# Kernel optimization log

Measured on AMD Instinct MI355X. Metric: run time of the kernel, lower is better.

Reference implementation:

```python
import jax, jax.numpy as jnp
import numpy as np

B, D, H = 8192, 512, 512


def _linear_init(key, out_dim, in_dim, bias=True):
    # torch nn.Linear default: U(-1/sqrt(in_dim), 1/sqrt(in_dim)) for W and b
    k1, k2 = jax.random.split(key)
    bound = 1.0 / np.sqrt(in_dim)
    W = jax.random.uniform(k1, (out_dim, in_dim), jnp.float32, -bound, bound)
    if not bias:
        return W
    b = jax.random.uniform(k2, (out_dim,), jnp.float32, -bound, bound)
    return W, b


def setup_inputs() -> dict:
    key = jax.random.key(0)
    ks = jax.random.split(key, 16)
    x = jax.random.normal(ks[0], (B, D), jnp.float32)
    delta_t = jax.random.uniform(ks[1], (B, 1), jnp.float32)
    hidden = jax.random.normal(ks[2], (B, H), jnp.float32)
    cell_s = jax.random.normal(ks[3], (B, H), jnp.float32)
    Wii, bii = _linear_init(ks[4], H, D)
    Whi, bhi = _linear_init(ks[5], H, H)
    Wig, big = _linear_init(ks[6], H, D)
    Whg, bhg = _linear_init(ks[7], H, H)
    Wio, bio = _linear_init(ks[8], H, D)
    Who, bho = _linear_init(ks[9], H, H)
    Wto, bto = _linear_init(ks[10], H, 1)
    Wco, bco = _linear_init(ks[11], H, H)
    Wit1, bit1 = _linear_init(ks[12], H, D)
    Wtt1 = _linear_init(ks[13], H, 1, bias=False)
    Wit2, bit2 = _linear_init(ks[14], H, D)
    Wtt2 = _linear_init(ks[15], H, 1, bias=False)
    return dict(x=x, delta_t=delta_t, hidden=hidden, cell_s=cell_s,
                Wii=Wii, bii=bii, Whi=Whi, bhi=bhi, Wig=Wig, big=big,
                Whg=Whg, bhg=bhg, Wio=Wio, bio=bio, Who=Who, bho=bho,
                Wto=Wto, bto=bto, Wco=Wco, bco=bco, Wit1=Wit1, bit1=bit1,
                Wtt1=Wtt1, Wit2=Wit2, bit2=bit2, Wtt2=Wtt2)


def _lin(a, W, b=None):
    y = a @ W.T
    return y if b is None else y + b


def reference(x, delta_t, hidden, cell_s,
              Wii, bii, Whi, bhi, Wig, big, Whg, bhg,
              Wio, bio, Who, bho, Wto, bto, Wco, bco,
              Wit1, bit1, Wtt1, Wit2, bit2, Wtt2):
    sig, tanh = jax.nn.sigmoid, jnp.tanh
    tm1 = sig(_lin(x, Wit1, bit1) + sig(_lin(delta_t, Wtt1)))
    tm2 = sig(_lin(x, Wit2, bit2) + sig(_lin(delta_t, Wtt2)))
    im = sig(_lin(x, Wii, bii) + _lin(hidden, Whi, bhi))
    cur_in = tanh(_lin(x, Wig, big) + _lin(hidden, Whg, bhg))
    it1 = im * tm1
    cm_t = (1.0 - it1) * cell_s + it1 * cur_in
    cm = (1.0 - im) * cell_s + im * tm2 * cur_in
    om = sig(_lin(x, Wio, bio) + _lin(delta_t, Wto, bto)
             + _lin(hidden, Who, bho) + _lin(cm_t, Wco, bco))
    hm = om * tanh(cm_t)
    return (hm, cm)
```

## Files before the change

kernel.cpp:

```cpp
#include <hip/hip_runtime.h>
#include <hip/hip_bf16.h>
#include <stdint.h>

#define B_SZ 8192
#define D_SZ 512
#define H_SZ 512
#define KC 1024
#define NPRE 2560
#define PRE_LD 2560

typedef __attribute__((ext_vector_type(8))) __bf16 bf16x8;
typedef __attribute__((ext_vector_type(4))) float f32x4;

__device__ __forceinline__ unsigned short f2bf(float f) {
  unsigned u = __builtin_bit_cast(unsigned, f);
  u += 0x7FFFu + ((u >> 16) & 1u);
  return (unsigned short)(u >> 16);
}
__device__ __forceinline__ float bf2f(unsigned short h) {
  unsigned u = ((unsigned)h) << 16;
  return __builtin_bit_cast(float, u);
}
__device__ __forceinline__ float sigf(float x) { return 1.0f / (1.0f + __expf(-x)); }

__device__ __forceinline__ void async_ld16(const unsigned short* g, unsigned short* l) {
  __builtin_amdgcn_global_load_lds(
      (const __attribute__((address_space(1))) unsigned int*)g,
      (__attribute__((address_space(3))) unsigned int*)l, 16, 0, 0);
}

struct WSrcs { const float* wx[5]; const float* wh[3]; const float* wco; };

__global__ void pack_all(const float* __restrict__ x, const float* __restrict__ h, WSrcs ws,
                         unsigned short* __restrict__ Ab, unsigned short* __restrict__ Wall,
                         unsigned short* __restrict__ Wcob) {
  int i = (blockIdx.x * 256 + threadIdx.x) * 4;
  const int XH = B_SZ * KC;
  const float* s;
  unsigned short* d;
  if (i < XH) {
    int b = i >> 10, c = i & 1023;
    s = (c < 512) ? (x + (size_t)b * 512 + c) : (h + (size_t)b * 512 + (c - 512));
    d = Ab + i;
  } else if (i < XH + NPRE * KC) {
    int j = i - XH;
    int row = j >> 10, c = j & 1023;
    int gate = row >> 9, r = row & 511;
    d = Wall + j;
    if (c < 512) {
      s = ws.wx[gate] + (size_t)r * 512 + c;
    } else if (gate >= 2) {
      s = ws.wh[gate - 2] + (size_t)r * 512 + (c - 512);
    } else {
      *(ushort4*)d = (ushort4){0, 0, 0, 0};
      return;
    }
  } else {
    int j = i - XH - NPRE * KC;
    s = ws.wco + j;
    d = Wcob + j;
  }
  float4 v = *(const float4*)s;
  ushort4 o; o.x = f2bf(v.x); o.y = f2bf(v.y); o.z = f2bf(v.z); o.w = f2bf(v.w);
  *(ushort4*)d = o;
}

__global__ __launch_bounds__(256, 2) void gemm_bt(
    const unsigned short* __restrict__ A, const unsigned short* __restrict__ W,
    unsigned short* __restrict__ C, int K, int ldc) {
  __shared__ bf16x8 sA[128 * 8];
  __shared__ bf16x8 sW[128 * 8];
  const int tid  = threadIdx.x;
  const int wave = tid >> 6, lane = tid & 63;
  const int ln15 = lane & 15, kq = lane >> 4;
  const int wr = wave >> 1, wc = wave & 1;
  const long bm = (long)blockIdx.y * 128;
  const long bn = (long)blockIdx.x * 128;

  f32x4 acc[4][4];
#pragma unroll
  for (int i = 0; i < 4; ++i)
#pragma unroll
    for (int j = 0; j < 4; ++j) acc[i][j] = (f32x4){0.f, 0.f, 0.f, 0.f};

  const int nK = (bn < 1024) ? (512 >> 6) : (K >> 6);
  const int swb = ln15 & 7;

  for (int kt = 0; kt < nK; ++kt) {
    const int k0 = kt << 6;
    __syncthreads();
#pragma unroll
    for (int it = 0; it < 4; ++it) {
      int f   = it * 256 + tid;
      int row = f >> 3;
      int col = ((f & 7) ^ (row & 7)) << 3;
      int ldsc = it * 256 + wave * 64;
      async_ld16(A + (size_t)(bm + row) * K + k0 + col, (unsigned short*)sA + (size_t)ldsc * 8);
      async_ld16(W + (size_t)(bn + row) * K + k0 + col, (unsigned short*)sW + (size_t)ldsc * 8);
    }
    __syncthreads();
#pragma unroll
    for (int ko = 0; ko < 2; ++ko) {
      const int q = (ko * 4 + kq) ^ swb;
      bf16x8 af[4], wf[4];
#pragma unroll
      for (int t = 0; t < 4; ++t)
        af[t] = sA[(wr * 64 + t * 16 + ln15) * 8 + q];
#pragma unroll
      for (int t = 0; t < 4; ++t)
        wf[t] = sW[(wc * 64 + t * 16 + ln15) * 8 + q];
#pragma unroll
      for (int i = 0; i < 4; ++i)
#pragma unroll
        for (int j = 0; j < 4; ++j)
          acc[i][j] = __builtin_amdgcn_mfma_f32_16x16x32_bf16(af[i], wf[j], acc[i][j], 0, 0, 0);
    }
  }
#pragma unroll
  for (int i = 0; i < 4; ++i) {
    const long r0 = bm + wr * 64 + i * 16 + kq * 4;
#pragma unroll
    for (int j = 0; j < 4; ++j) {
      const long c = bn + wc * 64 + j * 16 + ln15;
#pragma unroll
      for (int r = 0; r < 4; ++r)
        C[(size_t)(r0 + r) * ldc + c] = f2bf(acc[i][j][r]);
    }
  }
}

__global__ void gate_kernel(unsigned short* __restrict__ Pre,
                            const float* __restrict__ delta_t, const float* __restrict__ cell_s,
                            const float* __restrict__ bii, const float* __restrict__ bhi,
                            const float* __restrict__ big, const float* __restrict__ bhg,
                            const float* __restrict__ bio, const float* __restrict__ bho,
                            const float* __restrict__ Wto, const float* __restrict__ bto,
                            const float* __restrict__ bco,
                            const float* __restrict__ bit1, const float* __restrict__ Wtt1,
                            const float* __restrict__ bit2, const float* __restrict__ Wtt2,
                            float* __restrict__ out_cm, unsigned short* __restrict__ cmt_b) {
  int i4 = (blockIdx.x * 256 + threadIdx.x) * 4;
  int b = i4 >> 9, h = i4 & 511;
  size_t p = (size_t)b * PRE_LD;
  float dt = delta_t[b];
  ushort4 u1 = *(const ushort4*)(Pre + p + h);
  ushort4 u2 = *(const ushort4*)(Pre + p + 512 + h);
  ushort4 ui = *(const ushort4*)(Pre + p + 1024 + h);
  ushort4 ug = *(const ushort4*)(Pre + p + 1536 + h);
  ushort4 uo = *(const ushort4*)(Pre + p + 2048 + h);
  float4 cs  = *(const float4*)(cell_s + i4);
  float4 vbii = *(const float4*)(bii + h),  vbhi = *(const float4*)(bhi + h);
  float4 vbig = *(const float4*)(big + h),  vbhg = *(const float4*)(bhg + h);
  float4 vbio = *(const float4*)(bio + h),  vbho = *(const float4*)(bho + h);
  float4 vWto = *(const float4*)(Wto + h),  vbto = *(const float4*)(bto + h);
  float4 vbco = *(const float4*)(bco + h);
  float4 vbt1 = *(const float4*)(bit1 + h), vwt1 = *(const float4*)(Wtt1 + h);
  float4 vbt2 = *(const float4*)(bit2 + h), vwt2 = *(const float4*)(Wtt2 + h);

  float4 ocm; ushort4 ocmt; ushort4 oao;
  const unsigned short* pu1 = (const unsigned short*)&u1;
  const unsigned short* pu2 = (const unsigned short*)&u2;
  const unsigned short* pui = (const unsigned short*)&ui;
  const unsigned short* pug = (const unsigned short*)&ug;
  const unsigned short* puo = (const unsigned short*)&uo;
  const float* pcs = (const float*)&cs;
  float* pocm = (float*)&ocm;
  unsigned short* pocmt = (unsigned short*)&ocmt;
  unsigned short* poao = (unsigned short*)&oao;
#pragma unroll
  for (int l = 0; l < 4; ++l) {
    float a1 = bf2f(pu1[l]) + ((const float*)&vbt1)[l];
    float a2 = bf2f(pu2[l]) + ((const float*)&vbt2)[l];
    float ai = bf2f(pui[l]) + ((const float*)&vbii)[l] + ((const float*)&vbhi)[l];
    float ag = bf2f(pug[l]) + ((const float*)&vbig)[l] + ((const float*)&vbhg)[l];
    float ao = bf2f(puo[l]) + ((const float*)&vbio)[l] + ((const float*)&vbho)[l]
             + dt * ((const float*)&vWto)[l] + ((const float*)&vbto)[l] + ((const float*)&vbco)[l];
    float t1 = sigf(a1 + sigf(dt * ((const float*)&vwt1)[l]));
    float t2 = sigf(a2 + sigf(dt * ((const float*)&vwt2)[l]));
    float im = sigf(ai);
    float g  = tanhf(ag);
    float csl = pcs[l];
    float it1 = im * t1;
    float cmt = (1.f - it1) * csl + it1 * g;
    float cm  = (1.f - im) * csl + im * t2 * g;
    pocm[l]  = cm;
    pocmt[l] = f2bf(cmt);
    poao[l]  = f2bf(ao);
  }
  *(float4*)(out_cm + i4) = ocm;
  *(ushort4*)(cmt_b + i4) = ocmt;
  *(ushort4*)(Pre + p + 2048 + h) = oao;
}

__global__ __launch_bounds__(256, 2) void gemm_out(
    const unsigned short* __restrict__ A , const unsigned short* __restrict__ W ,
    const unsigned short* __restrict__ Pre, float* __restrict__ out_hm) {
  __shared__ bf16x8 sA[128 * 8];
  __shared__ bf16x8 sW[128 * 8];
  const int tid  = threadIdx.x;
  const int wave = tid >> 6, lane = tid & 63;
  const int ln15 = lane & 15, kq = lane >> 4;
  const int wr = wave >> 1, wc = wave & 1;
  const long bm = (long)blockIdx.y * 128;
  const long bn = (long)blockIdx.x * 128;
  const int K = H_SZ;
  const int swb = ln15 & 7;

  f32x4 acc[4][4];
#pragma unroll
  for (int i = 0; i < 4; ++i)
#pragma unroll
    for (int j = 0; j < 4; ++j) acc[i][j] = (f32x4){0.f, 0.f, 0.f, 0.f};

  for (int kt = 0; kt < (K >> 6); ++kt) {
    const int k0 = kt << 6;
    __syncthreads();
#pragma unroll
    for (int it = 0; it < 4; ++it) {
      int f   = it * 256 + tid;
      int row = f >> 3;
      int col = ((f & 7) ^ (row & 7)) << 3;
      int ldsc = it * 256 + wave * 64;
      async_ld16(A + (size_t)(bm + row) * K + k0 + col, (unsigned short*)sA + (size_t)ldsc * 8);
      async_ld16(W + (size_t)(bn + row) * K + k0 + col, (unsigned short*)sW + (size_t)ldsc * 8);
    }
    __syncthreads();
#pragma unroll
    for (int ko = 0; ko < 2; ++ko) {
      const int q = (ko * 4 + kq) ^ swb;
      bf16x8 af[4], wf[4];
#pragma unroll
      for (int t = 0; t < 4; ++t)
        af[t] = sA[(wr * 64 + t * 16 + ln15) * 8 + q];
#pragma unroll
      for (int t = 0; t < 4; ++t)
        wf[t] = sW[(wc * 64 + t * 16 + ln15) * 8 + q];
#pragma unroll
      for (int i = 0; i < 4; ++i)
#pragma unroll
        for (int j = 0; j < 4; ++j)
          acc[i][j] = __builtin_amdgcn_mfma_f32_16x16x32_bf16(af[i], wf[j], acc[i][j], 0, 0, 0);
    }
  }
#pragma unroll
  for (int i = 0; i < 4; ++i) {
    const long r0 = bm + wr * 64 + i * 16 + kq * 4;
#pragma unroll
    for (int j = 0; j < 4; ++j) {
      const long c = bn + wc * 64 + j * 16 + ln15;
#pragma unroll
      for (int r = 0; r < 4; ++r) {
        long row = r0 + r;
        size_t idx = (size_t)row * H_SZ + c;
        float ao  = bf2f(Pre[(size_t)row * PRE_LD + 2048 + c]);
        float om  = sigf(ao + acc[i][j][r]);
        float cmt = bf2f(A[idx]);
        out_hm[idx] = om * tanhf(cmt);
      }
    }
  }
}

extern "C" void kernel_launch(void* const* d_in, const int* in_sizes, int n_in,
                              void* d_out, int out_size, void* d_ws, size_t ws_size,
                              hipStream_t stream) {
  const float* x    = (const float*)d_in[0];
  const float* dt   = (const float*)d_in[1];
  const float* hid  = (const float*)d_in[2];
  const float* cell = (const float*)d_in[3];
  const float* Wii  = (const float*)d_in[4];
  const float* bii  = (const float*)d_in[5];
  const float* Whi  = (const float*)d_in[6];
  const float* bhi  = (const float*)d_in[7];
  const float* Wig  = (const float*)d_in[8];
  const float* big  = (const float*)d_in[9];
  const float* Whg  = (const float*)d_in[10];
  const float* bhg  = (const float*)d_in[11];
  const float* Wio  = (const float*)d_in[12];
  const float* bio  = (const float*)d_in[13];
  const float* Who  = (const float*)d_in[14];
  const float* bho  = (const float*)d_in[15];
  const float* Wto  = (const float*)d_in[16];
  const float* bto  = (const float*)d_in[17];
  const float* Wco  = (const float*)d_in[18];
  const float* bco  = (const float*)d_in[19];
  const float* Wit1 = (const float*)d_in[20];
  const float* bit1 = (const float*)d_in[21];
  const float* Wtt1 = (const float*)d_in[22];
  const float* Wit2 = (const float*)d_in[23];
  const float* bit2 = (const float*)d_in[24];
  const float* Wtt2 = (const float*)d_in[25];

  char* wp = (char*)d_ws;
  unsigned short* Ab   = (unsigned short*)wp; wp += (size_t)B_SZ * KC * 2;
  unsigned short* Wall = (unsigned short*)wp; wp += (size_t)NPRE * KC * 2;
  unsigned short* Wcob = (unsigned short*)wp; wp += (size_t)H_SZ * H_SZ * 2;
  unsigned short* Pre  = (unsigned short*)wp; wp += (size_t)B_SZ * PRE_LD * 2;
  unsigned short* Cmtb = (unsigned short*)wp; wp += (size_t)B_SZ * H_SZ * 2;

  float* out = (float*)d_out;

  WSrcs wsrc;
  wsrc.wx[0] = Wit1; wsrc.wx[1] = Wit2; wsrc.wx[2] = Wii; wsrc.wx[3] = Wig; wsrc.wx[4] = Wio;
  wsrc.wh[0] = Whi;  wsrc.wh[1] = Whg;  wsrc.wh[2] = Who; wsrc.wco = Wco;
  const int pack_elems = B_SZ * KC + NPRE * KC + H_SZ * H_SZ;
  pack_all<<<pack_elems / 4 / 256, 256, 0, stream>>>(x, hid, wsrc, Ab, Wall, Wcob);

  gemm_bt<<<dim3(NPRE / 128, B_SZ / 128), 256, 0, stream>>>(Ab, Wall, Pre, KC, PRE_LD);

  gate_kernel<<<(B_SZ * H_SZ) / 4 / 256, 256, 0, stream>>>(
      Pre, dt, cell, bii, bhi, big, bhg, bio, bho, Wto, bto, bco, bit1, Wtt1, bit2, Wtt2,
      out + (size_t)B_SZ * H_SZ, Cmtb);

  gemm_out<<<dim3(H_SZ / 128, B_SZ / 128), 256, 0, stream>>>(Cmtb, Wcob, Pre, out);
}
```

Measured before the change: 233.9 us.

## Fuse gate elementwise into GEMMs, split T1/T2 and i/g/o gate GEMMs

The time-gate sigmoids move into the epilogue of a K=512 GEMM that writes T12. The input, cell and output gate GEMMs are computed together in a new 384-thread kernel that stages three 64-column weight tiles plus a 128-row A tile in LDS. That kernel applies the gate math in its epilogue, which removes the separate gate_kernel and the round trip through the wide Pre buffer. Zero-filling the unused weight half is dropped because T1/T2 now only read the first 512 K. The trade-off is larger LDS use and a non-power-of-two block shape that may lower occupancy.

```diff
diff --git a/kernel.cpp b/kernel.cpp
--- a/kernel.cpp
+++ b/kernel.cpp
@@ -7,7 +7,6 @@
 #define H_SZ 512
 #define KC 1024
 #define NPRE 2560
-#define PRE_LD 2560
 
 typedef __attribute__((ext_vector_type(8))) __bf16 bf16x8;
 typedef __attribute__((ext_vector_type(4))) float f32x4;
@@ -52,7 +51,6 @@
     } else if (gate >= 2) {
       s = ws.wh[gate - 2] + (size_t)r * 512 + (c - 512);
     } else {
-      *(ushort4*)d = (ushort4){0, 0, 0, 0};
       return;
     }
   } else {
@@ -65,9 +63,12 @@
   *(ushort4*)d = o;
 }
 
-__global__ __launch_bounds__(256, 2) void gemm_bt(
+__global__ __launch_bounds__(256, 2) void gemm_t12(
     const unsigned short* __restrict__ A, const unsigned short* __restrict__ W,
-    unsigned short* __restrict__ C, int K, int ldc) {
+    unsigned short* __restrict__ T12,
+    const float* __restrict__ bit1, const float* __restrict__ Wtt1,
+    const float* __restrict__ bit2, const float* __restrict__ Wtt2,
+    const float* __restrict__ delta_t) {
   __shared__ bf16x8 sA[128 * 8];
   __shared__ bf16x8 sW[128 * 8];
   const int tid  = threadIdx.x;
@@ -83,10 +84,8 @@
 #pragma unroll
     for (int j = 0; j < 4; ++j) acc[i][j] = (f32x4){0.f, 0.f, 0.f, 0.f};
 
-  const int nK = (bn < 1024) ? (512 >> 6) : (K >> 6);
   const int swb = ln15 & 7;
-
-  for (int kt = 0; kt < nK; ++kt) {
+  for (int kt = 0; kt < 8; ++kt) {
     const int k0 = kt << 6;
     __syncthreads();
 #pragma unroll
@@ -95,8 +94,8 @@
       int row = f >> 3;
       int col = ((f & 7) ^ (row & 7)) << 3;
       int ldsc = it * 256 + wave * 64;
-      async_ld16(A + (size_t)(bm + row) * K + k0 + col, (unsigned short*)sA + (size_t)ldsc * 8);
-      async_ld16(W + (size_t)(bn + row) * K + k0 + col, (unsigned short*)sW + (size_t)ldsc * 8);
+      async_ld16(A + (size_t)(bm + row) * KC + k0 + col, (unsigned short*)sA + (size_t)ldsc * 8);
+      async_ld16(W + (size_t)(bn + row) * KC + k0 + col, (unsigned short*)sW + (size_t)ldsc * 8);
     }
     __syncthreads();
 #pragma unroll
@@ -116,85 +115,151 @@
           acc[i][j] = __builtin_amdgcn_mfma_f32_16x16x32_bf16(af[i], wf[j], acc[i][j], 0, 0, 0);
     }
   }
+  const float* bitp = (bn < 512) ? bit1 : bit2;
+  const float* wttp = (bn < 512) ? Wtt1 : Wtt2;
 #pragma unroll
   for (int i = 0; i < 4; ++i) {
     const long r0 = bm + wr * 64 + i * 16 + kq * 4;
 #pragma unroll
     for (int j = 0; j < 4; ++j) {
       const long c = bn + wc * 64 + j * 16 + ln15;
-#pragma unroll
-      for (int r = 0; r < 4; ++r)
-        C[(size_t)(r0 + r) * ldc + c] = f2bf(acc[i][j][r]);
-    }
-  }
-}
-
-__global__ void gate_kernel(unsigned short* __restrict__ Pre,
-                            const float* __restrict__ delta_t, const float* __restrict__ cell_s,
-                            const float* __restrict__ bii, const float* __restrict__ bhi,
-                            const float* __restrict__ big, const float* __restrict__ bhg,
-                            const float* __restrict__ bio, const float* __restrict__ bho,
-                            const float* __restrict__ Wto, const float* __restrict__ bto,
-                            const float* __restrict__ bco,
-                            const float* __restrict__ bit1, const float* __restrict__ Wtt1,
-                            const float* __restrict__ bit2, const float* __restrict__ Wtt2,
-                            float* __restrict__ out_cm, unsigned short* __restrict__ cmt_b) {
-  int i4 = (blockIdx.x * 256 + threadIdx.x) * 4;
-  int b = i4 >> 9, h = i4 & 511;
-  size_t p = (size_t)b * PRE_LD;
-  float dt = delta_t[b];
-  ushort4 u1 = *(const ushort4*)(Pre + p + h);
-  ushort4 u2 = *(const ushort4*)(Pre + p + 512 + h);
-  ushort4 ui = *(const ushort4*)(Pre + p + 1024 + h);
-  ushort4 ug = *(const ushort4*)(Pre + p + 1536 + h);
-  ushort4 uo = *(const ushort4*)(Pre + p + 2048 + h);
-  float4 cs  = *(const float4*)(cell_s + i4);
-  float4 vbii = *(const float4*)(bii + h),  vbhi = *(const float4*)(bhi + h);
-  float4 vbig = *(const float4*)(big + h),  vbhg = *(const float4*)(bhg + h);
-  float4 vbio = *(const float4*)(bio + h),  vbho = *(const float4*)(bho + h);
-  float4 vWto = *(const float4*)(Wto + h),  vbto = *(const float4*)(bto + h);
-  float4 vbco = *(const float4*)(bco + h);
-  float4 vbt1 = *(const float4*)(bit1 + h), vwt1 = *(const float4*)(Wtt1 + h);
-  float4 vbt2 = *(const float4*)(bit2 + h), vwt2 = *(const float4*)(Wtt2 + h);
-
-  float4 ocm; ushort4 ocmt; ushort4 oao;
-  const unsigned short* pu1 = (const unsigned short*)&u1;
-  const unsigned short* pu2 = (const unsigned short*)&u2;
-  const unsigned short* pui = (const unsigned short*)&ui;
-  const unsigned short* pug = (const unsigned short*)&ug;
-  const unsigned short* puo = (const unsigned short*)&uo;
-  const float* pcs = (const float*)&cs;
-  float* pocm = (float*)&ocm;
-  unsigned short* pocmt = (unsigned short*)&ocmt;
-  unsigned short* poao = (unsigned short*)&oao;
-#pragma unroll
-  for (int l = 0; l < 4; ++l) {
-    float a1 = bf2f(pu1[l]) + ((const float*)&vbt1)[l];
-    float a2 = bf2f(pu2[l]) + ((const float*)&vbt2)[l];
-    float ai = bf2f(pui[l]) + ((const float*)&vbii)[l] + ((const float*)&vbhi)[l];
-    float ag = bf2f(pug[l]) + ((const float*)&vbig)[l] + ((const float*)&vbhg)[l];
-    float ao = bf2f(puo[l]) + ((const float*)&vbio)[l] + ((const float*)&vbho)[l]
-             + dt * ((const float*)&vWto)[l] + ((const float*)&vbto)[l] + ((const float*)&vbco)[l];
-    float t1 = sigf(a1 + sigf(dt * ((const float*)&vwt1)[l]));
-    float t2 = sigf(a2 + sigf(dt * ((const float*)&vwt2)[l]));
-    float im = sigf(ai);
-    float g  = tanhf(ag);
-    float csl = pcs[l];
-    float it1 = im * t1;
-    float cmt = (1.f - it1) * csl + it1 * g;
-    float cm  = (1.f - im) * csl + im * t2 * g;
-    pocm[l]  = cm;
-    pocmt[l] = f2bf(cmt);
-    poao[l]  = f2bf(ao);
-  }
-  *(float4*)(out_cm + i4) = ocm;
-  *(ushort4*)(cmt_b + i4) = ocmt;
-  *(ushort4*)(Pre + p + 2048 + h) = oao;
+      const int hc = (int)c & 511;
+      const float bv = bitp[hc], wv = wttp[hc];
+#pragma unroll
+      for (int r = 0; r < 4; ++r) {
+        const long row = r0 + r;
+        float v = sigf(acc[i][j][r] + bv + sigf(delta_t[row] * wv));
+        T12[(size_t)row * 1024 + c] = f2bf(v);
+      }
+    }
+  }
+}
+
+__global__ __launch_bounds__(384, 2) void igo_gate(
+    const unsigned short* __restrict__ A, const unsigned short* __restrict__ Wigo,
+    const unsigned short* __restrict__ T12,
+    const float* __restrict__ delta_t, const float* __restrict__ cell_s,
+    const float* __restrict__ bii, const float* __restrict__ bhi,
+    const float* __restrict__ big, const float* __restrict__ bhg,
+    const float* __restrict__ bio, const float* __restrict__ bho,
+    const float* __restrict__ Wto, const float* __restrict__ bto,
+    const float* __restrict__ bco,
+    float* __restrict__ out_cm, unsigned short* __restrict__ cmt_b,
+    unsigned short* __restrict__ ao_b) {
+  __shared__ __align__(16) unsigned short sBuf[24576];
+  const int tid  = threadIdx.x;
+  const int wave = tid >> 6, lane = tid & 63;
+  const int ln15 = lane & 15, kq = lane >> 4;
+  const int mh   = wave / 3, slot = wave % 3;
+  const long bm  = (long)blockIdx.y * 128;
+  const int  bn64 = blockIdx.x * 64;
+
+  f32x4 acc[4][4];
+#pragma unroll
+  for (int i = 0; i < 4; ++i)
+#pragma unroll
+    for (int j = 0; j < 4; ++j) acc[i][j] = (f32x4){0.f, 0.f, 0.f, 0.f};
+
+  const int swb = ln15 & 7;
+  bf16x8* chunks = (bf16x8*)sBuf;
+
+  for (int kt = 0; kt < 16; ++kt) {
+    const int k0 = kt << 6;
+    __syncthreads();
+#pragma unroll
+    for (int it = 0; it < 7; ++it) {
+      int idx = it * 384 + tid;
+      if (idx < 2560) {
+        int t   = idx >> 9;
+        int f   = idx & 511;
+        int row = f >> 3;
+        int col = ((f & 7) ^ (row & 7)) << 3;
+        const unsigned short* src;
+        if (t < 2) src = A    + (size_t)(bm + t * 64 + row) * KC + k0 + col;
+        else       src = Wigo + (size_t)((t - 2) * 512 + bn64 + row) * KC + k0 + col;
+        async_ld16(src, sBuf + (size_t)idx * 8);
+      }
+    }
+    __syncthreads();
+#pragma unroll
+    for (int ko = 0; ko < 2; ++ko) {
+      const int q = (ko * 4 + kq) ^ swb;
+      bf16x8 af[4], wf[4];
+#pragma unroll
+      for (int t = 0; t < 4; ++t)
+        af[t] = chunks[mh * 512 + (t * 16 + ln15) * 8 + q];
+#pragma unroll
+      for (int t = 0; t < 4; ++t)
+        wf[t] = chunks[(2 + slot) * 512 + (t * 16 + ln15) * 8 + q];
+#pragma unroll
+      for (int i = 0; i < 4; ++i)
+#pragma unroll
+        for (int j = 0; j < 4; ++j)
+          acc[i][j] = __builtin_amdgcn_mfma_f32_16x16x32_bf16(af[i], wf[j], acc[i][j], 0, 0, 0);
+    }
+  }
+
+  __syncthreads();
+#pragma unroll
+  for (int i = 0; i < 4; ++i)
+#pragma unroll
+    for (int j = 0; j < 4; ++j)
+#pragma unroll
+      for (int r = 0; r < 4; ++r) {
+        int row = i * 16 + kq * 4 + r;
+        int col = j * 16 + ln15;
+        sBuf[(size_t)(mh * 3 + slot) * 4096 + row * 64 + col] = f2bf(acc[i][j][r]);
+      }
+  __syncthreads();
+
+  for (int e4 = tid * 4; e4 < 8192; e4 += 384 * 4) {
+    int emh = e4 >> 12;
+    int rc  = e4 & 4095;
+    int row = rc >> 6;
+    int col = rc & 63;
+    long b  = bm + emh * 64 + row;
+    int  h  = bn64 + col;
+    ushort4 uai = *(const ushort4*)(sBuf + (size_t)(emh * 3 + 0) * 4096 + row * 64 + col);
+    ushort4 uag = *(const ushort4*)(sBuf + (size_t)(emh * 3 + 1) * 4096 + row * 64 + col);
+    ushort4 uao = *(const ushort4*)(sBuf + (size_t)(emh * 3 + 2) * 4096 + row * 64 + col);
+    ushort4 ut1 = *(const ushort4*)(T12 + (size_t)b * 1024 + h);
+    ushort4 ut2 = *(const ushort4*)(T12 + (size_t)b * 1024 + 512 + h);
+    float4 cs   = *(const float4*)(cell_s + (size_t)b * 512 + h);
+    float4 vbii = *(const float4*)(bii + h), vbhi = *(const float4*)(bhi + h);
+    float4 vbig = *(const float4*)(big + h), vbhg = *(const float4*)(bhg + h);
+    float4 vbio = *(const float4*)(bio + h), vbho = *(const float4*)(bho + h);
+    float4 vWto = *(const float4*)(Wto + h), vbto = *(const float4*)(bto + h);
+    float4 vbco = *(const float4*)(bco + h);
+    float dtb   = delta_t[b];
+
+    float4 ocm; ushort4 ocmt, oao;
+#pragma unroll
+    for (int l = 0; l < 4; ++l) {
+      float ai = bf2f(((const unsigned short*)&uai)[l]) + ((const float*)&vbii)[l] + ((const float*)&vbhi)[l];
+      float ag = bf2f(((const unsigned short*)&uag)[l]) + ((const float*)&vbig)[l] + ((const float*)&vbhg)[l];
+      float ao = bf2f(((const unsigned short*)&uao)[l]) + ((const float*)&vbio)[l] + ((const float*)&vbho)[l]
+               + dtb * ((const float*)&vWto)[l] + ((const float*)&vbto)[l] + ((const float*)&vbco)[l];
+      float t1 = bf2f(((const unsigned short*)&ut1)[l]);
+      float t2 = bf2f(((const unsigned short*)&ut2)[l]);
+      float im = sigf(ai);
+      float g  = tanhf(ag);
+      float csl = ((const float*)&cs)[l];
+      float it1 = im * t1;
+      float cmt = (1.f - it1) * csl + it1 * g;
+      float cm  = (1.f - im) * csl + im * t2 * g;
+      ((float*)&ocm)[l] = cm;
+      ((unsigned short*)&ocmt)[l] = f2bf(cmt);
+      ((unsigned short*)&oao)[l]  = f2bf(ao);
+    }
+    *(float4*)(out_cm + (size_t)b * 512 + h) = ocm;
+    *(ushort4*)(cmt_b + (size_t)b * 512 + h) = ocmt;
+    *(ushort4*)(ao_b  + (size_t)b * 512 + h) = oao;
+  }
 }
 
 __global__ __launch_bounds__(256, 2) void gemm_out(
     const unsigned short* __restrict__ A , const unsigned short* __restrict__ W ,
-    const unsigned short* __restrict__ Pre, float* __restrict__ out_hm) {
+    const unsigned short* __restrict__ AO, float* __restrict__ out_hm) {
   __shared__ bf16x8 sA[128 * 8];
   __shared__ bf16x8 sW[128 * 8];
   const int tid  = threadIdx.x;
@@ -203,7 +268,6 @@
   const int wr = wave >> 1, wc = wave & 1;
   const long bm = (long)blockIdx.y * 128;
   const long bn = (long)blockIdx.x * 128;
-  const int K = H_SZ;
   const int swb = ln15 & 7;
 
   f32x4 acc[4][4];
@@ -212,7 +276,7 @@
 #pragma unroll
     for (int j = 0; j < 4; ++j) acc[i][j] = (f32x4){0.f, 0.f, 0.f, 0.f};
 
-  for (int kt = 0; kt < (K >> 6); ++kt) {
+  for (int kt = 0; kt < 8; ++kt) {
     const int k0 = kt << 6;
     __syncthreads();
 #pragma unroll
@@ -221,8 +285,8 @@
       int row = f >> 3;
       int col = ((f & 7) ^ (row & 7)) << 3;
       int ldsc = it * 256 + wave * 64;
-      async_ld16(A + (size_t)(bm + row) * K + k0 + col, (unsigned short*)sA + (size_t)ldsc * 8);
-      async_ld16(W + (size_t)(bn + row) * K + k0 + col, (unsigned short*)sW + (size_t)ldsc * 8);
+      async_ld16(A + (size_t)(bm + row) * H_SZ + k0 + col, (unsigned short*)sA + (size_t)ldsc * 8);
+      async_ld16(W + (size_t)(bn + row) * H_SZ + k0 + col, (unsigned short*)sW + (size_t)ldsc * 8);
     }
     __syncthreads();
 #pragma unroll
@@ -252,7 +316,7 @@
       for (int r = 0; r < 4; ++r) {
         long row = r0 + r;
         size_t idx = (size_t)row * H_SZ + c;
-        float ao  = bf2f(Pre[(size_t)row * PRE_LD + 2048 + c]);
+        float ao  = bf2f(AO[idx]);
         float om  = sigf(ao + acc[i][j][r]);
         float cmt = bf2f(A[idx]);
         out_hm[idx] = om * tanhf(cmt);
@@ -295,8 +359,9 @@
   unsigned short* Ab   = (unsigned short*)wp; wp += (size_t)B_SZ * KC * 2;
   unsigned short* Wall = (unsigned short*)wp; wp += (size_t)NPRE * KC * 2;
   unsigned short* Wcob = (unsigned short*)wp; wp += (size_t)H_SZ * H_SZ * 2;
-  unsigned short* Pre  = (unsigned short*)wp; wp += (size_t)B_SZ * PRE_LD * 2;
+  unsigned short* T12  = (unsigned short*)wp; wp += (size_t)B_SZ * 1024 * 2;
   unsigned short* Cmtb = (unsigned short*)wp; wp += (size_t)B_SZ * H_SZ * 2;
+  unsigned short* AOb  = (unsigned short*)wp; wp += (size_t)B_SZ * H_SZ * 2;
 
   float* out = (float*)d_out;
 
@@ -306,11 +371,12 @@
   const int pack_elems = B_SZ * KC + NPRE * KC + H_SZ * H_SZ;
   pack_all<<<pack_elems / 4 / 256, 256, 0, stream>>>(x, hid, wsrc, Ab, Wall, Wcob);
 
-  gemm_bt<<<dim3(NPRE / 128, B_SZ / 128), 256, 0, stream>>>(Ab, Wall, Pre, KC, PRE_LD);
-
-  gate_kernel<<<(B_SZ * H_SZ) / 4 / 256, 256, 0, stream>>>(
-      Pre, dt, cell, bii, bhi, big, bhg, bio, bho, Wto, bto, bco, bit1, Wtt1, bit2, Wtt2,
-      out + (size_t)B_SZ * H_SZ, Cmtb);
-
-  gemm_out<<<dim3(H_SZ / 128, B_SZ / 128), 256, 0, stream>>>(Cmtb, Wcob, Pre, out);
-}
+  gemm_t12<<<dim3(8, 64), 256, 0, stream>>>(Ab, Wall, T12, bit1, Wtt1, bit2, Wtt2, dt);
+
+  const unsigned short* Wigo = Wall + (size_t)1024 * KC;
+  igo_gate<<<dim3(8, 64), 384, 0, stream>>>(
+      Ab, Wigo, T12, dt, cell, bii, bhi, big, bhg, bio, bho, Wto, bto, bco,
+      out + (size_t)B_SZ * H_SZ, Cmtb, AOb);
+
+  gemm_out<<<dim3(4, 64), 256, 0, stream>>>(Cmtb, Wcob, AOb, out);
+}
```

After: 226.6 us. 3.1% less time.
